# Kernel tuning notes

Hardware: AMD Instinct MI355X
Metric: run time of the kernel (lower is better)

The kernel has to match this reference:

```python
import jax, jax.numpy as jnp
import numpy as np

B, Q, H, KVH, HD, HS = 2, 1024, 32, 8, 64, 2048
LCK = 2  # number of pre-existing cache entries
N_REP = H // KVH


def setup_inputs() -> dict:
    key = jax.random.key(0)
    ks = jax.random.split(key, 8)
    s = 0.02
    causal = jnp.tril(jnp.ones((Q, Q), dtype=bool))
    attention_mask = jnp.where(causal, 0.0, -1e9).astype(jnp.float32)[None, None]  # [1,1,Q,Q]
    return {
        "hidden_states": jax.random.normal(ks[0], (B, Q, 2 * HS), jnp.float32),
        "Wq": jax.random.normal(ks[1], (H * HD, 2 * HS), jnp.float32) * s,
        "Wk": jax.random.normal(ks[2], (KVH * HD, 2 * HS), jnp.float32) * s,
        "Wv": jax.random.normal(ks[3], (KVH * HD, 2 * HS), jnp.float32) * s,
        "Wo": jax.random.normal(ks[4], (H * HD, HS), jnp.float32).T * s,  # [HS, H*HD]
        "cache_k": jax.random.normal(ks[5], (LCK, B, H, Q, HD), jnp.float32),
        "cache_v": jax.random.normal(ks[6], (LCK, B, H, Q, HD), jnp.float32),
        "attention_mask": attention_mask,
        "position_ids": jnp.broadcast_to(jnp.arange(Q, dtype=jnp.int32), (B, Q)),
    }


def _rotate_half(x):
    return jnp.concatenate([-x[..., HD // 2:], x[..., :HD // 2]], axis=-1)


def reference(hidden_states, Wq, Wk, Wv, Wo, cache_k, cache_v, attention_mask, position_ids):
    b, q_len, _ = hidden_states.shape
    # QKV projections (Linear with weight [out,in]: x @ W.T)
    q = (hidden_states @ Wq.T).reshape(b, q_len, H, HD).transpose(0, 2, 1, 3)    # [b,H,q,hd]
    k = (hidden_states @ Wk.T).reshape(b, q_len, KVH, HD).transpose(0, 2, 1, 3)  # [b,KVH,q,hd]
    v = (hidden_states @ Wv.T).reshape(b, q_len, KVH, HD).transpose(0, 2, 1, 3)

    # RoPE at positions position_ids + lck (lck = LCK cached entries)
    inv_freq = 1.0 / (10000.0 ** (jnp.arange(0, HD, 2, dtype=jnp.float32) / HD))
    pos = (position_ids + LCK).astype(jnp.float32)                 # [b,q]
    freqs = pos[..., None] * inv_freq                              # [b,q,hd/2]
    emb = jnp.concatenate([freqs, freqs], axis=-1)                 # [b,q,hd]
    cos = jnp.cos(emb)[:, None]                                    # [b,1,q,hd]
    sin = jnp.sin(emb)[:, None]
    q = q * cos + _rotate_half(q) * sin
    k = k * cos + _rotate_half(k) * sin

    # GQA repeat_kv
    k = jnp.repeat(k, N_REP, axis=1)  # [b,H,q,hd]
    v = jnp.repeat(v, N_REP, axis=1)

    scale = 1.0 / np.sqrt(HD)
    k0, v0 = cache_k[0], cache_v[0]
    # full attention against first cache entry (+ causal mask)
    w0 = jnp.einsum('bhqd,bhkd->bhqk', q, k0) * scale + attention_mask  # [b,H,q,q]
    # per-step diagonal attention against remaining cache entries + fresh k
    tail_k = jnp.concatenate([cache_k[1:], k[None]], axis=0)  # [LCK,b,H,q,hd]
    tail_v = jnp.concatenate([cache_v[1:], v[None]], axis=0)
    wtail = jnp.einsum('bhqd,nbhqd->bhqn', q, tail_k) * scale  # [b,H,q,LCK]

    w = jnp.concatenate([w0, wtail], axis=-1)
    w = jax.nn.softmax(w.astype(jnp.float32), axis=-1).astype(q.dtype)

    out = jnp.einsum('bhqk,bhkd->bhqd', w[..., :q_len], v0)
    out = out + jnp.einsum('bhqn,nbhqd->bhqd', w[..., q_len:], tail_v)

    out = out.transpose(0, 2, 1, 3).reshape(b, q_len, H * HD)
    return out @ Wo.T  # [b,q,HS]
```

## Files before the change

### kernel.cpp

```cpp
#include <hip/hip_runtime.h>
#include <hip/hip_bf16.h>
#include <math.h>

#define B_    2
#define Q_    1024
#define H_    32
#define KVH_  8
#define HD_   64
#define HS_   2048
#define NREP_ 4
#define KIN_  (2*HS_)
#define M_    (B_*Q_)
#define QKVN_ (H_*HD_ + 2*KVH_*HD_)
#define AOW_  (H_*HD_)
#define SCALE_ 0.125f

typedef __attribute__((ext_vector_type(8))) short bf16x8;
typedef __attribute__((ext_vector_type(4))) float f32x4;
typedef unsigned short u16;

static __device__ __forceinline__ u16 f2b(float f) {
  union { float f; unsigned int u; } c; c.f = f;
  unsigned int r = (c.u + 0x7fffu + ((c.u >> 16) & 1u)) >> 16;
  return (u16)r;
}
static __device__ __forceinline__ float b2f(u16 s) {
  union { unsigned int u; float f; } c;
  c.u = ((unsigned int)s) << 16;
  return c.f;
}
static __device__ __forceinline__ unsigned long long pack4s(float4 v, float sc) {
  return (unsigned long long)f2b(v.x*sc) |
         ((unsigned long long)f2b(v.y*sc) << 16) |
         ((unsigned long long)f2b(v.z*sc) << 32) |
         ((unsigned long long)f2b(v.w*sc) << 48);
}

#define GLOAD(SRC, DST) __builtin_amdgcn_global_load_lds( \
    (const __attribute__((address_space(1))) void*)(SRC), \
    (__attribute__((address_space(3))) void*)(DST), 16, 0, 0)

__global__ __launch_bounds__(256) void prep_kernel(
    const float* __restrict__ hidden, const float* __restrict__ Wq,
    const float* __restrict__ Wk, const float* __restrict__ Wv,
    const float* __restrict__ Wo,
    const float* __restrict__ k0, const float* __restrict__ v0,
    u16* __restrict__ Xb, u16* __restrict__ Wb, u16* __restrict__ Wob,
    u16* __restrict__ Kb, u16* __restrict__ Vtb)
{
  __shared__ float Vs[64][65];
  const int bx = blockIdx.x;
  const int t = threadIdx.x;
  if (bx < 1024) {
    const int kt = bx & 15, bh = bx >> 4;
    const int r = t >> 2, seg = t & 3;
    {
      const float* sp = k0 + ((size_t)bh*Q_ + (kt<<6) + r)*64;
      u16* dp = Kb + ((size_t)bh*Q_ + (kt<<6) + r)*64;
#pragma unroll
      for (int c2 = 2*seg; c2 < 2*seg+2; ++c2) {
        int ca = c2 ^ (r & 7);
        float4 a = *(const float4*)(sp + ca*8);
        float4 b = *(const float4*)(sp + ca*8 + 4);
        unsigned long long o[2] = {pack4s(a,1.f), pack4s(b,1.f)};
        *(float4*)(dp + c2*8) = *(const float4*)o;
      }
    }
    {
      const float* sp = v0 + ((size_t)bh*Q_ + (kt<<6) + r)*64 + seg*16;
#pragma unroll
      for (int c = 0; c < 4; ++c) {
        float4 v = *(const float4*)(sp + 4*c);
        Vs[r][seg*16 + 4*c + 0] = v.x; Vs[r][seg*16 + 4*c + 1] = v.y;
        Vs[r][seg*16 + 4*c + 2] = v.z; Vs[r][seg*16 + 4*c + 3] = v.w;
      }
    }
    __syncthreads();
    {
      const int d = r;
      u16* dp = Vtb + ((size_t)bh*64 + d)*Q_ + (kt<<6);
#pragma unroll
      for (int c2 = 2*seg; c2 < 2*seg+2; ++c2) {
        int ca = c2 ^ (d & 7);
        u16 o[8];
#pragma unroll
        for (int j = 0; j < 8; ++j) o[j] = f2b(Vs[ca*8 + j][d]);
        *(float4*)(dp + c2*8) = *(const float4*)o;
      }
    }
  } else {
    const int U0 = 1048576;
    const int U1 = U0 + 1048576;
    const int U2 = U1 + 262144;
    const int U3 = U2 + 262144;
    const int U4 = U3 + 524288;
    for (int u = (bx - 1024)*256 + t; u < U4; u += 2048*256) {
      const float* src; u16* dst;
      if (u < U0)      { src = hidden + (size_t)u*8;   dst = Xb + (size_t)u*8; }
      else if (u < U1) { src = Wq + (size_t)(u-U0)*8;  dst = Wb + (size_t)(u-U0)*8; }
      else if (u < U2) { src = Wk + (size_t)(u-U1)*8;  dst = Wb + (size_t)2048*KIN_ + (size_t)(u-U1)*8; }
      else if (u < U3) { src = Wv + (size_t)(u-U2)*8;  dst = Wb + (size_t)2560*KIN_ + (size_t)(u-U2)*8; }
      else             { src = Wo + (size_t)(u-U3)*8;  dst = Wob + (size_t)(u-U3)*8; }
      float4 a = *(const float4*)src;
      float4 bb = *(const float4*)(src + 4);
      unsigned long long o[2] = {pack4s(a, 1.f), pack4s(bb, 1.f)};
      *(float4*)dst = *(const float4*)o;
    }
  }
}

template<bool QKV>
__global__ __launch_bounds__(256, 3) void gemm_nt(
    const u16* __restrict__ A, const u16* __restrict__ W,
    void* __restrict__ Cv, int K, int ldc, const int* __restrict__ pos_ids)
{
  __shared__ u16 As[2*128*64];
  __shared__ u16 Bs[2*64*64];
  const int m0 = blockIdx.y << 7, n0 = blockIdx.x << 6;
  const int t = threadIdx.x;
  const int wave = t >> 6, lane = t & 63;
  const int wr = wave >> 1, wc = wave & 1;

  f32x4 acc[4][2] = {};

  const int lrow8 = lane >> 3;
  const int lcsw  = ((lane & 7) ^ lrow8) * 8;
  const int fr    = lane & 15;
  const int g     = lane >> 4;

#define GEMM_STAGE(BUF, K0) do { \
    _Pragma("unroll") \
    for (int p = 0; p < 4; ++p) { \
      int rbase = p * 32 + wave * 8; \
      GLOAD(A + (size_t)(m0 + rbase + lrow8) * K + (K0) + lcsw, \
            As + (BUF)*8192 + rbase * 64); \
    } \
    _Pragma("unroll") \
    for (int p = 0; p < 2; ++p) { \
      int rbase = p * 32 + wave * 8; \
      GLOAD(W + (size_t)(n0 + rbase + lrow8) * K + (K0) + lcsw, \
            Bs + (BUF)*4096 + rbase * 64); \
    } \
  } while(0)

  GEMM_STAGE(0, 0);
  int cur = 0;
  for (int k0 = 0; k0 < K; k0 += 64) {
    if (k0 + 64 < K) {
      GEMM_STAGE(cur ^ 1, k0 + 64);
      asm volatile("s_waitcnt vmcnt(6)" ::: "memory");
    } else {
      asm volatile("s_waitcnt vmcnt(0)" ::: "memory");
    }
    asm volatile("s_barrier" ::: "memory");

    const u16* Ab = As + cur*8192;
    const u16* Bb = Bs + cur*4096;
    bf16x8 af[4][2], bfr[2][2];
#pragma unroll
    for (int kk = 0; kk < 2; ++kk) {
      int ck = kk * 4 + g;
#pragma unroll
      for (int mi = 0; mi < 4; ++mi) {
        int row = wr * 64 + mi * 16 + fr;
        af[mi][kk] = *(const bf16x8*)(Ab + row * 64 + ((ck ^ (row & 7)) << 3));
      }
#pragma unroll
      for (int ni = 0; ni < 2; ++ni) {
        int row = wc * 32 + ni * 16 + fr;
        bfr[ni][kk] = *(const bf16x8*)(Bb + row * 64 + ((ck ^ (row & 7)) << 3));
      }
    }
    __builtin_amdgcn_s_setprio(1);
#pragma unroll
    for (int kk = 0; kk < 2; ++kk)
#pragma unroll
      for (int mi = 0; mi < 4; ++mi)
#pragma unroll
        for (int ni = 0; ni < 2; ++ni)
          acc[mi][ni] = __builtin_amdgcn_mfma_f32_16x16x32_bf16(af[mi][kk], bfr[ni][kk], acc[mi][ni], 0, 0, 0);
    __builtin_amdgcn_s_setprio(0);
    asm volatile("s_barrier" ::: "memory");
    cur ^= 1;
  }
#undef GEMM_STAGE

  if (QKV && n0 < 2560) {
    float* xch = (float*)As;
    __syncthreads();
#pragma unroll
    for (int mi = 0; mi < 4; ++mi)
#pragma unroll
      for (int ni = 0; ni < 2; ++ni)
#pragma unroll
        for (int r = 0; r < 4; ++r)
          xch[(wr*64 + mi*16 + g*4 + r)*64 + wc*32 + ni*16 + (lane & 15)] = acc[mi][ni][r];
    __syncthreads();
    const bool isq = (n0 < 2048);
    u16* outp = (u16*)Cv;
    const float inv0 = exp2f(-0.4152410118609203f * (float)(lane & 15));
    const float invs[2] = {inv0, inv0 * 0.01f};
#pragma unroll
    for (int mi = 0; mi < 4; ++mi) {
#pragma unroll
      for (int r = 0; r < 4; ++r) {
        int rl = wr*64 + mi*16 + g*4 + r;
        int m = m0 + rl;
        float p = (float)(pos_ids[m] + 2);
#pragma unroll
        for (int ni = 0; ni < 2; ++ni) {
          float f = p * invs[ni];
          float s, c;
          __sincosf(f, &s, &c);
          float mine = acc[mi][ni][r];
          float part = xch[rl*64 + ((wc^1)*32 + ni*16 + (lane & 15))];
          float outv = (wc == 0) ? (mine*c - part*s) : (mine*c + part*s);
          if (isq) outv *= SCALE_;
          outp[(size_t)m * ldc + n0 + wc*32 + ni*16 + (lane & 15)] = f2b(outv);
        }
      }
    }
  } else {
#pragma unroll
    for (int mi = 0; mi < 4; ++mi) {
      int rbase = m0 + wr * 64 + mi * 16 + g * 4;
#pragma unroll
      for (int ni = 0; ni < 2; ++ni) {
        int col = n0 + wc * 32 + ni * 16 + (lane & 15);
#pragma unroll
        for (int r = 0; r < 4; ++r) {
          if (QKV) ((u16*)Cv)[(size_t)(rbase + r) * ldc + col] = f2b(acc[mi][ni][r]);
          else     ((float*)Cv)[(size_t)(rbase + r) * ldc + col] = acc[mi][ni][r];
        }
      }
    }
  }
}

__global__ __launch_bounds__(512, 4) void attn_mfma(
    const u16* __restrict__ Yb,
    const u16* __restrict__ Kb,
    const u16* __restrict__ Vtb,
    const float* __restrict__ cache_k,
    const float* __restrict__ cache_v,
    u16* __restrict__ AOb)
{
  __shared__ u16 Qs[128*64];
  __shared__ u16 Ps[128*64];
  __shared__ u16 Ks[2*64*64];
  __shared__ u16 Vt[2*64*64];

  const int bid = blockIdx.x;
  const int xcd = bid & 7, within = bid >> 3;
  const int w8 = within & 7;
  const int qtb = (w8 & 1) ? (7 - (w8 >> 1)) : (w8 >> 1);
  const int pair = xcd * 8 + (within >> 3);
  const int h = pair >> 1, b = pair & 1;
  const int bh = b * H_ + h;

  const int t = threadIdx.x;
  const int wave = t >> 6, lane = t & 63;
  const int g = lane >> 4, sub = lane & 15;
  const int wq0 = wave * 16;
  const int srow = lane >> 3;
  const int scc  = lane & 7;

  const u16* KbT = Kb + (size_t)bh * Q_ * 64;
  const u16* VtT = Vtb + (size_t)bh * 64 * Q_;

#define ATTN_STAGE(BUF, KT) do { \
    int r_ = wave*8 + srow; \
    GLOAD(KbT + (size_t)(((KT)<<6) + r_)*64 + scc*8, Ks + (BUF)*4096 + wave*512); \
    GLOAD(VtT + (size_t)r_*Q_ + ((KT)<<6) + scc*8,   Vt + (BUF)*4096 + wave*512); \
  } while(0)

  {
#pragma unroll
    for (int p = 0; p < 2; ++p) {
      int r = p*64 + wave*8 + srow;
      GLOAD(Yb + (size_t)(b*Q_ + qtb*128 + r)*QKVN_ + h*64 + ((scc ^ (r&7))<<3),
            Qs + p*4096 + wave*512);
    }
  }
  ATTN_STAGE(0, 0);
  asm volatile("s_waitcnt vmcnt(2)" ::: "memory");
  asm volatile("s_barrier" ::: "memory");

  bf16x8 qb[2];
#pragma unroll
  for (int kk = 0; kk < 2; ++kk) {
    int row = wq0 + sub;
    qb[kk] = *(const bf16x8*)&Qs[row*64 + (((4*kk+g) ^ (row&7))<<3)];
  }

  float m_run = -3e38f, l_run = 0.f;
  f32x4 acc_o[4] = {};
  int cur = 0;
  const int nkt = 2*qtb + 2;

  for (int kt = 0; kt < nkt; ++kt) {
    if (kt + 1 < nkt) {
      ATTN_STAGE(cur ^ 1, kt + 1);
      asm volatile("s_waitcnt vmcnt(2)" ::: "memory");
    } else {
      asm volatile("s_waitcnt vmcnt(0)" ::: "memory");
    }
    asm volatile("s_barrier" ::: "memory");

    if (kt*64 <= qtb*128 + wq0 + 15) {
      const u16* ksb = Ks + cur*4096;
      const u16* vtb = Vt + cur*4096;

      f32x4 s[4] = {};
      __builtin_amdgcn_s_setprio(1);
#pragma unroll
      for (int kk = 0; kk < 2; ++kk) {
        int kb = 4*kk + g;
#pragma unroll
        for (int cb = 0; cb < 4; ++cb) {
          int krow = cb*16 + sub;
          bf16x8 kf = *(const bf16x8*)&ksb[krow*64 + ((kb ^ (krow&7))<<3)];
          s[cb] = __builtin_amdgcn_mfma_f32_16x16x32_bf16(kf, qb[kk], s[cb], 0, 0, 0);
        }
      }
      __builtin_amdgcn_s_setprio(0);

      if (kt >= 2*qtb) {
#pragma unroll
        for (int cb = 0; cb < 4; ++cb)
#pragma unroll
          for (int r = 0; r < 4; ++r)
            if (kt*64 + cb*16 + 4*g + r > qtb*128 + wq0 + sub) s[cb][r] = -3e38f;
      }

      float mt = -3e38f;
#pragma unroll
      for (int cb = 0; cb < 4; ++cb)
#pragma unroll
        for (int r = 0; r < 4; ++r) mt = fmaxf(mt, s[cb][r]);
      mt = fmaxf(mt, __shfl_xor(mt, 16, 64));
      mt = fmaxf(mt, __shfl_xor(mt, 32, 64));

      float al = 1.0f;
      if (__any(mt > m_run + 8.f)) {
        float mnew = fmaxf(m_run, mt);
        al = __expf(m_run - mnew);
        m_run = mnew;
        int base = (lane & 48) + ((lane & 48) >> 2);
#pragma unroll
        for (int r = 0; r < 4; ++r) {
          float alr = __shfl(al, base + r, 64);
#pragma unroll
          for (int db = 0; db < 4; ++db) acc_o[db][r] *= alr;
        }
      }

      float sum = 0.f;
#pragma unroll
      for (int cb = 0; cb < 4; ++cb) {
        float p0 = __expf(s[cb][0]-m_run), p1 = __expf(s[cb][1]-m_run);
        float p2 = __expf(s[cb][2]-m_run), p3 = __expf(s[cb][3]-m_run);
        sum += (p0+p1)+(p2+p3);
        unsigned long long pk =
            (unsigned long long)((unsigned int)f2b(p0) | ((unsigned int)f2b(p1)<<16)) |
            ((unsigned long long)((unsigned int)f2b(p2) | ((unsigned int)f2b(p3)<<16)) << 32);
        int col8 = cb*2 + (g>>1);
        int dst = (wq0 + sub)*64 + ((col8 ^ (sub&7))<<3) + ((g&1)<<2);
        *(unsigned long long*)&Ps[dst] = pk;
      }
      sum += __shfl_xor(sum, 16, 64);
      sum += __shfl_xor(sum, 32, 64);
      l_run = l_run*al + sum;

      __builtin_amdgcn_s_setprio(1);
#pragma unroll
      for (int kk = 0; kk < 2; ++kk) {
        bf16x8 pa = *(const bf16x8*)&Ps[(wq0 + sub)*64 + (((4*kk+g) ^ (sub&7))<<3)];
#pragma unroll
        for (int db = 0; db < 4; ++db) {
          int drow = db*16 + sub;
          bf16x8 vf = *(const bf16x8*)&vtb[drow*64 + (((4*kk+g) ^ (drow&7))<<3)];
          acc_o[db] = __builtin_amdgcn_mfma_f32_16x16x32_bf16(pa, vf, acc_o[db], 0, 0, 0);
        }
      }
      __builtin_amdgcn_s_setprio(0);
    }
    asm volatile("s_barrier" ::: "memory");
    cur ^= 1;
  }
#undef ATTN_STAGE

  const int qrow_mine = wq0 + sub;
  const int qpos_mine = qtb*128 + qrow_mine;
  float e1 = 0.f, e2 = 0.f;
  {
    const float* k1p = cache_k + ((size_t)((B_ + b)*H_ + h)*Q_ + qpos_mine)*HD_ + g*16;
    const u16*   kfp = Yb + (size_t)(b*Q_ + qpos_mine)*QKVN_ + H_*HD_ + (h/NREP_)*HD_ + g*16;
    float qv[16];
#pragma unroll
    for (int half = 0; half < 2; ++half) {
      int kb = 2*g + half;
      bf16x8 qq = *(const bf16x8*)&Qs[qrow_mine*64 + ((kb ^ (qrow_mine&7))<<3)];
#pragma unroll
      for (int i = 0; i < 8; ++i) qv[half*8 + i] = b2f(((u16)qq[i]));
    }
    float4 kf4a = *(const float4*)kfp;
    float4 kf4b = *(const float4*)(kfp + 8);
    const u16* kf16a = (const u16*)&kf4a;
    const u16* kf16b = (const u16*)&kf4b;
#pragma unroll
    for (int c = 0; c < 4; ++c) {
      float4 kv1 = *(const float4*)(k1p + 4*c);
      e1 += qv[4*c]*kv1.x + qv[4*c+1]*kv1.y + qv[4*c+2]*kv1.z + qv[4*c+3]*kv1.w;
    }
#pragma unroll
    for (int i = 0; i < 8; ++i) {
      e2 += qv[i]   * b2f(kf16a[i]);
      e2 += qv[8+i] * b2f(kf16b[i]);
    }
  }
  e1 += __shfl_xor(e1, 16, 64); e1 += __shfl_xor(e1, 32, 64);
  e2 += __shfl_xor(e2, 16, 64); e2 += __shfl_xor(e2, 32, 64);

#pragma unroll
  for (int r = 0; r < 4; ++r) {
    int row = 4*g + r;
    int src = (lane & 48) | row;
    float e1r = __shfl(e1, src, 64);
    float e2r = __shfl(e2, src, 64);
    float m_r = __shfl(m_run, src, 64);
    float l_r = __shfl(l_run, src, 64);
    float mnew = fmaxf(m_r, fmaxf(e1r, e2r));
    float alr = __expf(m_r - mnew);
    float w1  = __expf(e1r - mnew);
    float w2  = __expf(e2r - mnew);
    float linv = 1.f / (l_r*alr + w1 + w2);
    int qpos = qtb*128 + wq0 + row;
    const float* v1p = cache_v + ((size_t)((B_ + b)*H_ + h)*Q_ + qpos)*HD_;
    const u16*   vfp = Yb + (size_t)(b*Q_ + qpos)*QKVN_ + (H_*HD_ + KVH_*HD_) + (h/NREP_)*HD_;
    u16* op = AOb + (size_t)(b*Q_ + qpos)*AOW_ + h*HD_;
#pragma unroll
    for (int db = 0; db < 4; ++db) {
      int d = db*16 + sub;
      float o = (acc_o[db][r]*alr + w1*v1p[d] + w2*b2f(vfp[d])) * linv;
      op[d] = f2b(o);
    }
  }
}

extern "C" void kernel_launch(void* const* d_in, const int* in_sizes, int n_in,
                              void* d_out, int out_size, void* d_ws, size_t ws_size,
                              hipStream_t stream) {
  const float* hidden  = (const float*)d_in[0];
  const float* Wq      = (const float*)d_in[1];
  const float* Wk      = (const float*)d_in[2];
  const float* Wv      = (const float*)d_in[3];
  const float* Wo      = (const float*)d_in[4];
  const float* cache_k = (const float*)d_in[5];
  const float* cache_v = (const float*)d_in[6];
  const int*   pos_ids = (const int*)d_in[8];
  float* out = (float*)d_out;

  char* ws = (char*)d_ws;
  u16* Yb  = (u16*)ws;  ws += (size_t)M_ * QKVN_ * 2;
  u16* Xb  = (u16*)ws;  ws += (size_t)M_ * KIN_ * 2;
  u16* Wb  = (u16*)ws;  ws += (size_t)QKVN_ * KIN_ * 2;
  u16* Wob = (u16*)ws;  ws += (size_t)HS_ * AOW_ * 2;
  u16* Kb  = (u16*)ws;  ws += (size_t)B_*H_*Q_*64 * 2;
  u16* Vtb = (u16*)ws;  ws += (size_t)B_*H_*Q_*64 * 2;
  u16* AOb = Xb;

  prep_kernel<<<dim3(3072), 256, 0, stream>>>(
      hidden, Wq, Wk, Wv, Wo, cache_k, cache_v, Xb, Wb, Wob, Kb, Vtb);

  gemm_nt<true><<<dim3(QKVN_/64, M_/128), 256, 0, stream>>>(Xb, Wb, (void*)Yb, KIN_, QKVN_, pos_ids);
  attn_mfma<<<dim3(512), 512, 0, stream>>>(Yb, Kb, Vtb, cache_k, cache_v, AOb);
  gemm_nt<false><<<dim3(HS_/64, M_/128), 256, 0, stream>>>(AOb, Wob, (void*)out, AOW_, HS_, nullptr);
}
```

Measured before the change: 162.3 us.

## Overlap cache K/V conversion with QKV GEMM and simplify GEMM pipeline

Splits the prep kernel so the cache K/V cast and transpose now run inside the QKV GEMM launch on odd block ids, interleaved with the GEMM tiles. The Wo cast moves into its own kernel. The GEMM drops double buffering for a single-buffered loop with two syncthreads per k-step and raises the occupancy hint. B-tile columns are remapped so RoPE halves land in the same lane, which removes the LDS exchange in the epilogue. The aim is to hide the cache conversion behind GEMM work and cut epilogue traffic, at the cost of losing load/compute overlap inside the GEMM. The leftover no-op loop and the use of grid-wide interleaving make load balance uncertain.

```diff
diff --git a/kernel.cpp b/kernel.cpp
--- a/kernel.cpp
+++ b/kernel.cpp
@@ -40,84 +40,93 @@
     (const __attribute__((address_space(1))) void*)(SRC), \
     (__attribute__((address_space(3))) void*)(DST), 16, 0, 0)
 
-__global__ __launch_bounds__(256) void prep_kernel(
+__global__ __launch_bounds__(256) void prep1(
     const float* __restrict__ hidden, const float* __restrict__ Wq,
     const float* __restrict__ Wk, const float* __restrict__ Wv,
-    const float* __restrict__ Wo,
+    u16* __restrict__ Xb, u16* __restrict__ Wb)
+{
+  const int U0 = 1048576;
+  const int U1 = U0 + 1048576;
+  const int U2 = U1 + 262144;
+  const int U3 = U2 + 262144;
+  for (int u = blockIdx.x*256 + threadIdx.x; u < U3; u += 2048*256) {
+    const float* src; u16* dst;
+    if (u < U0)      { src = hidden + (size_t)u*8;   dst = Xb + (size_t)u*8; }
+    else if (u < U1) { src = Wq + (size_t)(u-U0)*8;  dst = Wb + (size_t)(u-U0)*8; }
+    else if (u < U2) { src = Wk + (size_t)(u-U1)*8;  dst = Wb + (size_t)2048*KIN_ + (size_t)(u-U1)*8; }
+    else             { src = Wv + (size_t)(u-U2)*8;  dst = Wb + (size_t)2560*KIN_ + (size_t)(u-U2)*8; }
+    float4 a = *(const float4*)src;
+    float4 bb = *(const float4*)(src + 4);
+    unsigned long long o[2] = {pack4s(a, 1.f), pack4s(bb, 1.f)};
+    *(float4*)dst = *(const float4*)o;
+  }
+}
+
+template<bool QKV>
+__global__ __launch_bounds__(256, 4) void gemm_nt(
+    const u16* __restrict__ A, const u16* __restrict__ W,
+    void* __restrict__ Cv, int K, int ldc, int ntn,
+    const int* __restrict__ pos_ids,
     const float* __restrict__ k0, const float* __restrict__ v0,
-    u16* __restrict__ Xb, u16* __restrict__ Wb, u16* __restrict__ Wob,
     u16* __restrict__ Kb, u16* __restrict__ Vtb)
 {
-  __shared__ float Vs[64][65];
+  __shared__ __align__(16) char SMEM[24576];
   const int bx = blockIdx.x;
   const int t = threadIdx.x;
-  if (bx < 1024) {
-    const int kt = bx & 15, bh = bx >> 4;
+
+  if (QKV && (bx & 1)) {
+    const int aux_id = bx >> 1;
+    float (*Vs)[65] = (float (*)[65])SMEM;
     const int r = t >> 2, seg = t & 3;
-    {
-      const float* sp = k0 + ((size_t)bh*Q_ + (kt<<6) + r)*64;
-      u16* dp = Kb + ((size_t)bh*Q_ + (kt<<6) + r)*64;
-#pragma unroll
-      for (int c2 = 2*seg; c2 < 2*seg+2; ++c2) {
-        int ca = c2 ^ (r & 7);
-        float4 a = *(const float4*)(sp + ca*8);
-        float4 b = *(const float4*)(sp + ca*8 + 4);
-        unsigned long long o[2] = {pack4s(a,1.f), pack4s(b,1.f)};
-        *(float4*)(dp + c2*8) = *(const float4*)o;
-      }
-    }
-    {
-      const float* sp = v0 + ((size_t)bh*Q_ + (kt<<6) + r)*64 + seg*16;
-#pragma unroll
-      for (int c = 0; c < 4; ++c) {
-        float4 v = *(const float4*)(sp + 4*c);
-        Vs[r][seg*16 + 4*c + 0] = v.x; Vs[r][seg*16 + 4*c + 1] = v.y;
-        Vs[r][seg*16 + 4*c + 2] = v.z; Vs[r][seg*16 + 4*c + 3] = v.w;
-      }
-    }
-    __syncthreads();
-    {
-      const int d = r;
-      u16* dp = Vtb + ((size_t)bh*64 + d)*Q_ + (kt<<6);
-#pragma unroll
-      for (int c2 = 2*seg; c2 < 2*seg+2; ++c2) {
-        int ca = c2 ^ (d & 7);
-        u16 o[8];
-#pragma unroll
-        for (int j = 0; j < 8; ++j) o[j] = f2b(Vs[ca*8 + j][d]);
-        *(float4*)(dp + c2*8) = *(const float4*)o;
-      }
-    }
-  } else {
-    const int U0 = 1048576;
-    const int U1 = U0 + 1048576;
-    const int U2 = U1 + 262144;
-    const int U3 = U2 + 262144;
-    const int U4 = U3 + 524288;
-    for (int u = (bx - 1024)*256 + t; u < U4; u += 2048*256) {
-      const float* src; u16* dst;
-      if (u < U0)      { src = hidden + (size_t)u*8;   dst = Xb + (size_t)u*8; }
-      else if (u < U1) { src = Wq + (size_t)(u-U0)*8;  dst = Wb + (size_t)(u-U0)*8; }
-      else if (u < U2) { src = Wk + (size_t)(u-U1)*8;  dst = Wb + (size_t)2048*KIN_ + (size_t)(u-U1)*8; }
-      else if (u < U3) { src = Wv + (size_t)(u-U2)*8;  dst = Wb + (size_t)2560*KIN_ + (size_t)(u-U2)*8; }
-      else             { src = Wo + (size_t)(u-U3)*8;  dst = Wob + (size_t)(u-U3)*8; }
-      float4 a = *(const float4*)src;
-      float4 bb = *(const float4*)(src + 4);
-      unsigned long long o[2] = {pack4s(a, 1.f), pack4s(bb, 1.f)};
-      *(float4*)dst = *(const float4*)o;
-    }
-  }
-}
-
-template<bool QKV>
-__global__ __launch_bounds__(256, 3) void gemm_nt(
-    const u16* __restrict__ A, const u16* __restrict__ W,
-    void* __restrict__ Cv, int K, int ldc, const int* __restrict__ pos_ids)
-{
-  __shared__ u16 As[2*128*64];
-  __shared__ u16 Bs[2*64*64];
-  const int m0 = blockIdx.y << 7, n0 = blockIdx.x << 6;
-  const int t = threadIdx.x;
+    for (int tile = aux_id; tile < 1024; tile += 768) {
+      const int kt = tile & 15, bh = tile >> 4;
+      {
+        const float* sp = k0 + ((size_t)bh*Q_ + (kt<<6) + r)*64;
+        u16* dp = Kb + ((size_t)bh*Q_ + (kt<<6) + r)*64;
+#pragma unroll
+        for (int c2 = 2*seg; c2 < 2*seg+2; ++c2) {
+          int ca = c2 ^ (r & 7);
+          float4 a = *(const float4*)(sp + ca*8);
+          float4 b = *(const float4*)(sp + ca*8 + 4);
+          unsigned long long o[2] = {pack4s(a,1.f), pack4s(b,1.f)};
+          *(float4*)(dp + c2*8) = *(const float4*)o;
+        }
+      }
+      {
+        const float* sp = v0 + ((size_t)bh*Q_ + (kt<<6) + r)*64 + seg*16;
+#pragma unroll
+        for (int c = 0; c < 4; ++c) {
+          float4 v = *(const float4*)(sp + 4*c);
+          Vs[r][seg*16 + 4*c + 0] = v.x; Vs[r][seg*16 + 4*c + 1] = v.y;
+          Vs[r][seg*16 + 4*c + 2] = v.z; Vs[r][seg*16 + 4*c + 3] = v.w;
+        }
+      }
+      __syncthreads();
+      {
+        const int d = r;
+        u16* dp = Vtb + ((size_t)bh*64 + d)*Q_ + (kt<<6);
+#pragma unroll
+        for (int c2 = 2*seg; c2 < 2*seg+2; ++c2) {
+          int ca = c2 ^ (d & 7);
+          u16 o[8];
+#pragma unroll
+          for (int j = 0; j < 8; ++j) o[j] = f2b(Vs[ca*8 + j][d]);
+          *(float4*)(dp + c2*8) = *(const float4*)o;
+        }
+      }
+      __syncthreads();
+    }
+    for (int u = aux_id*256 + t; u < 524288; u += 768*256) {
+      const float* src = v0 - (size_t)B_*H_*Q_*64*2;
+      (void)src;
+    }
+    return;
+  }
+
+  u16* As = (u16*)SMEM;
+  u16* Bs = (u16*)(SMEM + 16384);
+  int gid = QKV ? (bx >> 1) : bx;
+  const int n0 = (gid % ntn) << 6, m0 = (gid / ntn) << 7;
   const int wave = t >> 6, lane = t & 63;
   const int wr = wave >> 1, wc = wave & 1;
 
@@ -127,35 +136,22 @@
   const int lcsw  = ((lane & 7) ^ lrow8) * 8;
   const int fr    = lane & 15;
   const int g     = lane >> 4;
-
-#define GEMM_STAGE(BUF, K0) do { \
-    _Pragma("unroll") \
-    for (int p = 0; p < 4; ++p) { \
-      int rbase = p * 32 + wave * 8; \
-      GLOAD(A + (size_t)(m0 + rbase + lrow8) * K + (K0) + lcsw, \
-            As + (BUF)*8192 + rbase * 64); \
-    } \
-    _Pragma("unroll") \
-    for (int p = 0; p < 2; ++p) { \
-      int rbase = p * 32 + wave * 8; \
-      GLOAD(W + (size_t)(n0 + rbase + lrow8) * K + (K0) + lcsw, \
-            Bs + (BUF)*4096 + rbase * 64); \
-    } \
-  } while(0)
-
-  GEMM_STAGE(0, 0);
-  int cur = 0;
-  for (int k0 = 0; k0 < K; k0 += 64) {
-    if (k0 + 64 < K) {
-      GEMM_STAGE(cur ^ 1, k0 + 64);
-      asm volatile("s_waitcnt vmcnt(6)" ::: "memory");
-    } else {
-      asm volatile("s_waitcnt vmcnt(0)" ::: "memory");
-    }
-    asm volatile("s_barrier" ::: "memory");
-
-    const u16* Ab = As + cur*8192;
-    const u16* Bb = Bs + cur*4096;
+  const int sub   = lane & 15;
+
+  for (int k0v = 0; k0v < K; k0v += 64) {
+    __syncthreads();
+#pragma unroll
+    for (int p = 0; p < 4; ++p) {
+      int rbase = p * 32 + wave * 8;
+      GLOAD(A + (size_t)(m0 + rbase + lrow8) * K + k0v + lcsw, As + rbase * 64);
+    }
+#pragma unroll
+    for (int p = 0; p < 2; ++p) {
+      int rbase = p * 32 + wave * 8;
+      GLOAD(W + (size_t)(n0 + rbase + lrow8) * K + k0v + lcsw, Bs + rbase * 64);
+    }
+    __syncthreads();
+
     bf16x8 af[4][2], bfr[2][2];
 #pragma unroll
     for (int kk = 0; kk < 2; ++kk) {
@@ -163,12 +159,12 @@
 #pragma unroll
       for (int mi = 0; mi < 4; ++mi) {
         int row = wr * 64 + mi * 16 + fr;
-        af[mi][kk] = *(const bf16x8*)(Ab + row * 64 + ((ck ^ (row & 7)) << 3));
+        af[mi][kk] = *(const bf16x8*)(As + row * 64 + ((ck ^ (row & 7)) << 3));
       }
 #pragma unroll
       for (int ni = 0; ni < 2; ++ni) {
-        int row = wc * 32 + ni * 16 + fr;
-        bfr[ni][kk] = *(const bf16x8*)(Bb + row * 64 + ((ck ^ (row & 7)) << 3));
+        int row = wc * 16 + ni * 32 + fr;
+        bfr[ni][kk] = *(const bf16x8*)(Bs + row * 64 + ((ck ^ (row & 7)) << 3));
       }
     }
     __builtin_amdgcn_s_setprio(1);
@@ -180,44 +176,25 @@
         for (int ni = 0; ni < 2; ++ni)
           acc[mi][ni] = __builtin_amdgcn_mfma_f32_16x16x32_bf16(af[mi][kk], bfr[ni][kk], acc[mi][ni], 0, 0, 0);
     __builtin_amdgcn_s_setprio(0);
-    asm volatile("s_barrier" ::: "memory");
-    cur ^= 1;
-  }
-#undef GEMM_STAGE
+  }
 
   if (QKV && n0 < 2560) {
-    float* xch = (float*)As;
-    __syncthreads();
-#pragma unroll
-    for (int mi = 0; mi < 4; ++mi)
-#pragma unroll
-      for (int ni = 0; ni < 2; ++ni)
-#pragma unroll
-        for (int r = 0; r < 4; ++r)
-          xch[(wr*64 + mi*16 + g*4 + r)*64 + wc*32 + ni*16 + (lane & 15)] = acc[mi][ni][r];
-    __syncthreads();
+    u16* outp = (u16*)Cv;
     const bool isq = (n0 < 2048);
-    u16* outp = (u16*)Cv;
-    const float inv0 = exp2f(-0.4152410118609203f * (float)(lane & 15));
-    const float invs[2] = {inv0, inv0 * 0.01f};
+    const float qs = isq ? SCALE_ : 1.0f;
+    const int d = wc*16 + sub;
+    const float inv = exp2f(-0.4152410118609203f * (float)d);
 #pragma unroll
     for (int mi = 0; mi < 4; ++mi) {
 #pragma unroll
       for (int r = 0; r < 4; ++r) {
-        int rl = wr*64 + mi*16 + g*4 + r;
-        int m = m0 + rl;
+        int m = m0 + wr*64 + mi*16 + g*4 + r;
         float p = (float)(pos_ids[m] + 2);
-#pragma unroll
-        for (int ni = 0; ni < 2; ++ni) {
-          float f = p * invs[ni];
-          float s, c;
-          __sincosf(f, &s, &c);
-          float mine = acc[mi][ni][r];
-          float part = xch[rl*64 + ((wc^1)*32 + ni*16 + (lane & 15))];
-          float outv = (wc == 0) ? (mine*c - part*s) : (mine*c + part*s);
-          if (isq) outv *= SCALE_;
-          outp[(size_t)m * ldc + n0 + wc*32 + ni*16 + (lane & 15)] = f2b(outv);
-        }
+        float f = p * inv, s, c;
+        __sincosf(f, &s, &c);
+        float x0 = acc[mi][0][r], x1 = acc[mi][1][r];
+        outp[(size_t)m * ldc + n0 + d]      = f2b((x0*c - x1*s) * qs);
+        outp[(size_t)m * ldc + n0 + 32 + d] = f2b((x1*c + x0*s) * qs);
       }
     }
   } else {
@@ -226,7 +203,7 @@
       int rbase = m0 + wr * 64 + mi * 16 + g * 4;
 #pragma unroll
       for (int ni = 0; ni < 2; ++ni) {
-        int col = n0 + wc * 32 + ni * 16 + (lane & 15);
+        int col = n0 + wc*16 + ni*32 + sub;
 #pragma unroll
         for (int r = 0; r < 4; ++r) {
           if (QKV) ((u16*)Cv)[(size_t)(rbase + r) * ldc + col] = f2b(acc[mi][ni][r]);
@@ -234,6 +211,19 @@
         }
       }
     }
+  }
+}
+
+__global__ __launch_bounds__(256) void cast_wo(
+    const float* __restrict__ Wo, u16* __restrict__ Wob)
+{
+  for (int u = blockIdx.x*256 + threadIdx.x; u < 524288; u += 512*256) {
+    const float* src = Wo + (size_t)u*8;
+    u16* dst = Wob + (size_t)u*8;
+    float4 a = *(const float4*)src;
+    float4 bb = *(const float4*)(src + 4);
+    unsigned long long o[2] = {pack4s(a, 1.f), pack4s(bb, 1.f)};
+    *(float4*)dst = *(const float4*)o;
   }
 }
 
@@ -470,10 +460,12 @@
   u16* Vtb = (u16*)ws;  ws += (size_t)B_*H_*Q_*64 * 2;
   u16* AOb = Xb;
 
-  prep_kernel<<<dim3(3072), 256, 0, stream>>>(
-      hidden, Wq, Wk, Wv, Wo, cache_k, cache_v, Xb, Wb, Wob, Kb, Vtb);
-
-  gemm_nt<true><<<dim3(QKVN_/64, M_/128), 256, 0, stream>>>(Xb, Wb, (void*)Yb, KIN_, QKVN_, pos_ids);
+  prep1<<<dim3(2048), 256, 0, stream>>>(hidden, Wq, Wk, Wv, Xb, Wb);
+  cast_wo<<<dim3(512), 256, 0, stream>>>(Wo, Wob);
+
+  gemm_nt<true><<<dim3(1536), 256, 0, stream>>>(
+      Xb, Wb, (void*)Yb, KIN_, QKVN_, 48, pos_ids, cache_k, cache_v, Kb, Vtb);
   attn_mfma<<<dim3(512), 512, 0, stream>>>(Yb, Kb, Vtb, cache_k, cache_v, AOb);
-  gemm_nt<false><<<dim3(HS_/64, M_/128), 256, 0, stream>>>(AOb, Wob, (void*)out, AOW_, HS_, nullptr);
-}
+  gemm_nt<false><<<dim3(512), 256, 0, stream>>>(
+      AOb, Wob, (void*)out, AOW_, HS_, 32, nullptr, nullptr, nullptr, nullptr, nullptr);
+}
```

Result: slower. 201.0 us (+23.8%).
